# Optimization experiments

Hardware: AMD Instinct MI355X
Metric: run time of the kernel (lower is better)

## Reference

```python
import jax, jax.numpy as jnp
import numpy as np

B, IN, OUT, N, K = 2048, 4096, 4096, 64, 4  # batch, in_features, out_features, num_nodes, degree


def setup_inputs() -> dict:
    key = jax.random.key(0)
    k0, k1, k2, k3 = jax.random.split(key, 4)
    x = jax.random.normal(k0, (B, IN), dtype=jnp.float32)
    # kaiming-ish init for the linear weight
    W = jax.random.normal(k1, (OUT, IN), dtype=jnp.float32) * (1.0 / np.sqrt(IN))
    ecoeff = jax.random.uniform(k2, (N, N), dtype=jnp.float32, minval=0.1, maxval=0.5)
    phase = jax.random.uniform(k3, (N, N), dtype=jnp.float32, minval=0.0, maxval=2.0 * np.pi)
    tension = jnp.ones((N,), dtype=jnp.float32)
    # deterministic degree-K ring topology: paths[i] = [(i+1..i+K) % N]
    src = jnp.repeat(jnp.arange(N), K).astype(jnp.int32)            # [E]
    dst = ((src + jnp.tile(jnp.arange(1, K + 1), N)) % N).astype(jnp.int32)  # [E]
    return {"x": x, "W": W, "ecoeff": ecoeff, "phase": phase,
            "tension": tension, "src": src, "dst": dst}


def reference(x, W, ecoeff, phase, tension, src, dst):
    # EntangledConnectionLayer.forward
    b = x.shape[0]
    out_features = W.shape[0]
    n = tension.shape[0]
    opn = out_features // n  # out_per_node

    out = x @ W.T  # [B, OUT] == F.linear(x, weights)
    nodes = out.reshape(b, n, opn)  # [B, N, opn] node-sliced view of output

    # entangled_connection_function on a real signal:
    # real(sig * (1 + eps*exp(i*phi)) / (1 + tau_i*tau_j)) = sig*(1+eps*cos(phi))/(1+tau_i*tau_j)
    eps = ecoeff[src, dst]                    # [E]
    phi = phase[src, dst]                     # [E]
    tau = tension[src] * tension[dst]         # [E]
    scale = (1.0 + eps * jnp.cos(phi)) / (1.0 + tau)  # [E]

    contrib = nodes[:, src, :] * scale[None, :, None]  # [B, E, opn]
    entangled = jnp.zeros_like(nodes).at[:, dst, :].add(contrib)  # scatter-add over edges

    return out + 0.5 * entangled.reshape(b, out_features)
```

## Files before the change

### kernel.cpp

```cpp
#include <hip/hip_runtime.h>
#include <hip/hip_bf16.h>

#define TILE 128
#define BK 64

typedef __attribute__((ext_vector_type(8))) short bf16x8;
typedef __attribute__((ext_vector_type(4))) float f32x4;

__device__ __forceinline__ unsigned short f32_to_bf16(float f) {
    unsigned u = __float_as_uint(f);
    unsigned rounded = u + 0x7FFF + ((u >> 16) & 1);
    return (unsigned short)(rounded >> 16);
}
__device__ __forceinline__ float bf16_to_f32(unsigned short h) {
    return __uint_as_float(((unsigned)h) << 16);
}
__device__ __forceinline__ bool probe_f32(const void* tens) {
    return ((const unsigned short*)tens)[0] == 0;
}

__global__ __launch_bounds__(256)
void cast_x_kernel(const void* __restrict__ xv, unsigned short* __restrict__ xo,
                   const void* __restrict__ tens)
{
    const bool isF32 = probe_f32(tens);
    const size_t i = ((size_t)blockIdx.x * 256 + threadIdx.x) * 8;
    if (isF32) {
        const float4 a = *(const float4*)((const float*)xv + i);
        const float4 b = *(const float4*)((const float*)xv + i + 4);
        unsigned short p[8];
        p[0]=f32_to_bf16(a.x); p[1]=f32_to_bf16(a.y); p[2]=f32_to_bf16(a.z); p[3]=f32_to_bf16(a.w);
        p[4]=f32_to_bf16(b.x); p[5]=f32_to_bf16(b.y); p[6]=f32_to_bf16(b.z); p[7]=f32_to_bf16(b.w);
        *(bf16x8*)(xo + i) = *(const bf16x8*)p;
    } else {
        *(bf16x8*)(xo + i) = *(const bf16x8*)((const unsigned short*)xv + i);
    }
}

__global__ __launch_bounds__(256)
void wprime_kernel(const void* __restrict__ Wv,
                   const void* __restrict__ ecoeff, const void* __restrict__ phase,
                   const void* __restrict__ tens,
                   const int* __restrict__ srcIdx, const int* __restrict__ dstIdx,
                   unsigned short* __restrict__ Wp, int E, int K)
{
    constexpr int NODES = 64, CHUNK = 128, CAP = 8;
    __shared__ float buf[NODES * CHUNK];
    __shared__ int   cnt[NODES];
    __shared__ int   slist[NODES * CAP];
    __shared__ float clist[NODES * CAP];

    const bool isF32 = probe_f32(tens);
    const int tid = threadIdx.x;
    const int j   = blockIdx.x;
    const int k0  = blockIdx.y * CHUNK;

    if (tid < NODES) cnt[tid] = 0;
    __syncthreads();
    if (tid < E) {
        const int s = srcIdx[tid];
        const int d = dstIdx[tid];
        float eps, phi, ts, td;
        if (isF32) {
            eps = ((const float*)ecoeff)[s * NODES + d];
            phi = ((const float*)phase)[s * NODES + d];
            ts  = ((const float*)tens)[s];
            td  = ((const float*)tens)[d];
        } else {
            eps = bf16_to_f32(((const unsigned short*)ecoeff)[s * NODES + d]);
            phi = bf16_to_f32(((const unsigned short*)phase)[s * NODES + d]);
            ts  = bf16_to_f32(((const unsigned short*)tens)[s]);
            td  = bf16_to_f32(((const unsigned short*)tens)[d]);
        }
        const float coef = 0.5f * (1.0f + eps * __cosf(phi)) / (1.0f + ts * td);
        const int pos = atomicAdd(&cnt[d], 1);
        if (pos < CAP) { slist[d * CAP + pos] = s; clist[d * CAP + pos] = coef; }
    }

    if (isF32) {
        for (int idx = tid; idx < NODES * CHUNK / 4; idx += 256) {
            const int s = idx >> 5;
            const int p = idx & 31;
            const float4 v = *(const float4*)
                ((const float*)Wv + ((size_t)(s * 64 + j)) * K + k0 + p * 4);
            *(float4*)&buf[s * CHUNK + p * 4] = v;
        }
    } else {
        for (int idx = tid; idx < NODES * CHUNK / 4; idx += 256) {
            const int s = idx >> 5;
            const int p = idx & 31;
            const ushort4 v = *(const ushort4*)
                ((const unsigned short*)Wv + ((size_t)(s * 64 + j)) * K + k0 + p * 4);
            buf[s * CHUNK + p * 4 + 0] = bf16_to_f32(v.x);
            buf[s * CHUNK + p * 4 + 1] = bf16_to_f32(v.y);
            buf[s * CHUNK + p * 4 + 2] = bf16_to_f32(v.z);
            buf[s * CHUNK + p * 4 + 3] = bf16_to_f32(v.w);
        }
    }
    __syncthreads();

    const int kk = tid & (CHUNK - 1);
    const int dh = (tid >> 7) * 32;
#pragma unroll 4
    for (int dd = 0; dd < 32; ++dd) {
        const int d = dh + dd;
        float v = buf[d * CHUNK + kk];
        const int n = cnt[d] < CAP ? cnt[d] : CAP;
        for (int t = 0; t < n; ++t)
            v += clist[d * CAP + t] * buf[slist[d * CAP + t] * CHUNK + kk];
        Wp[((size_t)(d * 64 + j)) * K + k0 + kk] = f32_to_bf16(v);
    }
}

__global__ __launch_bounds__(256)
void gemm_ws_kernel(const unsigned short* __restrict__ A,
                    const unsigned short* __restrict__ B,
                    void* __restrict__ Cv, const void* __restrict__ tens,
                    int M, int N, int K)
{
    __shared__ __align__(16) unsigned short As[TILE * BK];
    __shared__ __align__(16) unsigned short Bs[TILE * BK];

    const bool isF32 = probe_f32(tens);
    const int tid  = threadIdx.x;
    const int lane = tid & 63;
    const int w    = tid >> 6;
    const int wm   = (w >> 1) * 64;
    const int wn   = (w & 1) * 64;
    const int m0   = blockIdx.y * TILE;
    const int n0   = blockIdx.x * TILE;

    f32x4 acc[4][4] = {};

    const int lrow = lane >> 3;
    const int lcol = (lane & 7) * 8;

    for (int k0 = 0; k0 < K; k0 += BK) {
#pragma unroll
        for (int t = 0; t < 4; ++t) {
            const int br = t * 32 + w * 8;
            const unsigned short* ga = A + (size_t)(m0 + br + lrow) * K + (k0 + lcol);
            const unsigned short* gb = B + (size_t)(n0 + br + lrow) * K + (k0 + lcol);
            __builtin_amdgcn_global_load_lds(
                (__attribute__((address_space(1))) const void*)ga,
                (__attribute__((address_space(3))) void*)&As[br * BK], 16, 0, 0);
            __builtin_amdgcn_global_load_lds(
                (__attribute__((address_space(1))) const void*)gb,
                (__attribute__((address_space(3))) void*)&Bs[br * BK], 16, 0, 0);
        }
        __syncthreads();

#pragma unroll
        for (int kk = 0; kk < BK; kk += 32) {
            const int rk = kk + (lane >> 4) * 8;
            const int rr = lane & 15;
            bf16x8 av[4], bv[4];
#pragma unroll
            for (int i = 0; i < 4; ++i)
                av[i] = *(const bf16x8*)&As[(wm + i * 16 + rr) * BK + rk];
#pragma unroll
            for (int i = 0; i < 4; ++i)
                bv[i] = *(const bf16x8*)&Bs[(wn + i * 16 + rr) * BK + rk];
#pragma unroll
            for (int mt = 0; mt < 4; ++mt)
#pragma unroll
                for (int nt = 0; nt < 4; ++nt)
                    acc[mt][nt] = __builtin_amdgcn_mfma_f32_16x16x32_bf16(
                        av[mt], bv[nt], acc[mt][nt], 0, 0, 0);
        }
        __syncthreads();
    }

    const int quad = (lane >> 4) * 4;
    const int col  = lane & 15;
#pragma unroll
    for (int mt = 0; mt < 4; ++mt)
#pragma unroll
        for (int nt = 0; nt < 4; ++nt)
#pragma unroll
            for (int r = 0; r < 4; ++r) {
                const size_t gr = (size_t)(m0 + wm + mt * 16 + quad + r);
                const size_t gc = (size_t)(n0 + wn + nt * 16 + col);
                const float v = acc[mt][nt][r];
                if (isF32) ((float*)Cv)[gr * N + gc] = v;
                else       ((unsigned short*)Cv)[gr * N + gc] = f32_to_bf16(v);
            }
}

__global__ __launch_bounds__(256)
void gemm_bt_kernel(const void* __restrict__ Av, const void* __restrict__ Bv,
                    void* __restrict__ Cv, const void* __restrict__ tens,
                    int M, int N, int K)
{
    __shared__ __align__(16) short As[TILE * BK];
    __shared__ __align__(16) short Bs[TILE * BK];

    const bool isF32 = probe_f32(tens);
    const int tid  = threadIdx.x;
    const int lane = tid & 63;
    const int w    = tid >> 6;
    const int wm   = (w >> 1) * 64;
    const int wn   = (w & 1) * 64;
    const int m0   = blockIdx.y * TILE;
    const int n0   = blockIdx.x * TILE;
    f32x4 acc[4][4] = {};
    const int lrow = lane >> 3;
    const int lcol = (lane & 7) * 8;

    for (int k0 = 0; k0 < K; k0 += BK) {
        if (!isF32) {
            const short* A = (const short*)Av;
            const short* B = (const short*)Bv;
#pragma unroll
            for (int t = 0; t < 4; ++t) {
                const int br = t * 32 + w * 8;
                const short* ga = A + (size_t)(m0 + br + lrow) * K + (k0 + lcol);
                const short* gb = B + (size_t)(n0 + br + lrow) * K + (k0 + lcol);
                __builtin_amdgcn_global_load_lds(
                    (__attribute__((address_space(1))) const void*)ga,
                    (__attribute__((address_space(3))) void*)&As[br * BK], 16, 0, 0);
                __builtin_amdgcn_global_load_lds(
                    (__attribute__((address_space(1))) const void*)gb,
                    (__attribute__((address_space(3))) void*)&Bs[br * BK], 16, 0, 0);
            }
        } else {
            const float* A = (const float*)Av;
            const float* B = (const float*)Bv;
#pragma unroll
            for (int t = 0; t < 4; ++t) {
                const int br = t * 32 + w * 8;
                const int row = br + lrow;
                const float* ga = A + (size_t)(m0 + row) * K + (k0 + lcol);
                const float* gb = B + (size_t)(n0 + row) * K + (k0 + lcol);
                float4 a0 = *(const float4*)(ga);
                float4 a1 = *(const float4*)(ga + 4);
                float4 b0 = *(const float4*)(gb);
                float4 b1 = *(const float4*)(gb + 4);
                short pa[8], pb[8];
                pa[0]=f32_to_bf16(a0.x); pa[1]=f32_to_bf16(a0.y);
                pa[2]=f32_to_bf16(a0.z); pa[3]=f32_to_bf16(a0.w);
                pa[4]=f32_to_bf16(a1.x); pa[5]=f32_to_bf16(a1.y);
                pa[6]=f32_to_bf16(a1.z); pa[7]=f32_to_bf16(a1.w);
                pb[0]=f32_to_bf16(b0.x); pb[1]=f32_to_bf16(b0.y);
                pb[2]=f32_to_bf16(b0.z); pb[3]=f32_to_bf16(b0.w);
                pb[4]=f32_to_bf16(b1.x); pb[5]=f32_to_bf16(b1.y);
                pb[6]=f32_to_bf16(b1.z); pb[7]=f32_to_bf16(b1.w);
                *(bf16x8*)&As[row * BK + lcol] = *(const bf16x8*)pa;
                *(bf16x8*)&Bs[row * BK + lcol] = *(const bf16x8*)pb;
            }
        }
        __syncthreads();
#pragma unroll
        for (int kk = 0; kk < BK; kk += 32) {
            const int rk = kk + (lane >> 4) * 8;
            const int rr = lane & 15;
            bf16x8 av[4], bv[4];
#pragma unroll
            for (int i = 0; i < 4; ++i)
                av[i] = *(const bf16x8*)&As[(wm + i * 16 + rr) * BK + rk];
#pragma unroll
            for (int i = 0; i < 4; ++i)
                bv[i] = *(const bf16x8*)&Bs[(wn + i * 16 + rr) * BK + rk];
#pragma unroll
            for (int mt = 0; mt < 4; ++mt)
#pragma unroll
                for (int nt = 0; nt < 4; ++nt)
                    acc[mt][nt] = __builtin_amdgcn_mfma_f32_16x16x32_bf16(
                        av[mt], bv[nt], acc[mt][nt], 0, 0, 0);
        }
        __syncthreads();
    }
    const int quad = (lane >> 4) * 4;
    const int col  = lane & 15;
#pragma unroll
    for (int mt = 0; mt < 4; ++mt)
#pragma unroll
        for (int nt = 0; nt < 4; ++nt)
#pragma unroll
            for (int r = 0; r < 4; ++r) {
                const size_t gr = (size_t)(m0 + wm + mt * 16 + quad + r);
                const size_t gc = (size_t)(n0 + wn + nt * 16 + col);
                const float v = acc[mt][nt][r];
                if (isF32) ((float*)Cv)[gr * N + gc] = v;
                else       ((unsigned short*)Cv)[gr * N + gc] = f32_to_bf16(v);
            }
}

__global__ __launch_bounds__(256)
void entangle_kernel(void* __restrict__ Cv,
                     const void* __restrict__ ecoeff,
                     const void* __restrict__ phase,
                     const void* __restrict__ tens,
                     const int* __restrict__ srcIdx,
                     const int* __restrict__ dstIdx,
                     int E)
{
    constexpr int NODES = 64, OPN = 64, FEAT = 4096, ROWS = 2, CAP = 8;
    __shared__ float rows[ROWS * FEAT];
    __shared__ int   cnt[NODES];
    __shared__ int   slist[NODES * CAP];
    __shared__ float clist[NODES * CAP];

    const bool isF32 = probe_f32(tens);
    const int tid = threadIdx.x;
    if (tid < NODES) cnt[tid] = 0;
    __syncthreads();

    if (tid < E) {
        const int s = srcIdx[tid];
        const int d = dstIdx[tid];
        float eps, phi, ts, td;
        if (isF32) {
            eps = ((const float*)ecoeff)[s * NODES + d];
            phi = ((const float*)phase)[s * NODES + d];
            ts  = ((const float*)tens)[s];
            td  = ((const float*)tens)[d];
        } else {
            eps = bf16_to_f32(((const unsigned short*)ecoeff)[s * NODES + d]);
            phi = bf16_to_f32(((const unsigned short*)phase)[s * NODES + d]);
            ts  = bf16_to_f32(((const unsigned short*)tens)[s]);
            td  = bf16_to_f32(((const unsigned short*)tens)[d]);
        }
        const float coef = 0.5f * (1.0f + eps * __cosf(phi)) / (1.0f + ts * td);
        const int pos = atomicAdd(&cnt[d], 1);
        if (pos < CAP) { slist[d * CAP + pos] = s; clist[d * CAP + pos] = coef; }
    }

    const size_t row0 = (size_t)blockIdx.x * ROWS;
    if (isF32) {
        const float4* g = (const float4*)((const float*)Cv + row0 * FEAT);
        float4* l = (float4*)rows;
        for (int i = tid; i < ROWS * FEAT / 4; i += 256) l[i] = g[i];
    } else {
        const ushort2* g = (const ushort2*)((const unsigned short*)Cv + row0 * FEAT);
        for (int i = tid; i < ROWS * FEAT / 2; i += 256) {
            const ushort2 u = g[i];
            rows[i * 2 + 0] = bf16_to_f32(u.x);
            rows[i * 2 + 1] = bf16_to_f32(u.y);
        }
    }
    __syncthreads();

    for (int c = 0; c < ROWS * FEAT / 256; ++c) {
        const int i = c * 256 + tid;
        const int r = i >> 12;
        const int o = i & (FEAT - 1);
        const int d = o >> 6;
        const int j = o & (OPN - 1);
        float v = rows[i];
        const int n = cnt[d] < CAP ? cnt[d] : CAP;
        for (int t = 0; t < n; ++t)
            v += clist[d * CAP + t] * rows[(r << 12) + slist[d * CAP + t] * OPN + j];
        if (isF32) ((float*)Cv)[(row0 + r) * FEAT + o] = v;
        else       ((unsigned short*)Cv)[(row0 + r) * FEAT + o] = f32_to_bf16(v);
    }
}

extern "C" void kernel_launch(void* const* d_in, const int* in_sizes, int n_in,
                              void* d_out, int out_size, void* d_ws, size_t ws_size,
                              hipStream_t stream)
{
    const void* x       = d_in[0];
    const void* W       = d_in[1];
    const void* ecoeff  = d_in[2];
    const void* phase   = d_in[3];
    const void* tension = d_in[4];
    const int*  src     = (const int*)d_in[5];
    const int*  dst     = (const int*)d_in[6];

    const int INF  = 4096;
    const int OUTF = 4096;
    const int M    = in_sizes[0] / INF;
    const int E    = in_sizes[5];

    dim3 grid(OUTF / TILE, M / TILE), block(256);
    const size_t needA = (size_t)M * INF * sizeof(unsigned short);
    const size_t needW = (size_t)OUTF * INF * sizeof(unsigned short);

    if (ws_size >= needA + needW) {
        unsigned short* xa = (unsigned short*)d_ws;
        unsigned short* wp = (unsigned short*)((char*)d_ws + needA);
        cast_x_kernel<<<dim3((M * INF) / (256 * 8)), block, 0, stream>>>(x, xa, tension);
        wprime_kernel<<<dim3(64, INF / 128), block, 0, stream>>>(
            W, ecoeff, phase, tension, src, dst, wp, E, INF);
        gemm_ws_kernel<<<grid, block, 0, stream>>>(xa, wp, d_out, tension, M, OUTF, INF);
    } else {
        gemm_bt_kernel<<<grid, block, 0, stream>>>(x, W, d_out, tension, M, OUTF, INF);
        entangle_kernel<<<dim3(M / 2), block, 0, stream>>>(
            d_out, ecoeff, phase, tension, src, dst, E);
    }
}
```

Before: 264.7 us.

## Fuse prep kernels, add split-K GEMM with atomics, swizzle LDS layout

Merges the x cast, W' construction and a new output-zeroing pass into one prep kernel launch. The GEMM is split along K into two halves on fp32 outputs, with results accumulated via atomicAdd into a zeroed output, to double the number of workgroups (512 instead of 256 tiles). LDS tiles now use an XOR swizzle on 16-byte columns to reduce bank conflicts on the MFMA operand reads. The risks are extra atomic traffic and zeroing writes on a 32 MB output, and run-to-run nondeterminism in float summation order.

Result: slower. 280.0 us (+5.8%).

```diff
diff --git a/kernel.cpp b/kernel.cpp
--- a/kernel.cpp
+++ b/kernel.cpp
@@ -20,29 +20,13 @@
 }
 
 __global__ __launch_bounds__(256)
-void cast_x_kernel(const void* __restrict__ xv, unsigned short* __restrict__ xo,
-                   const void* __restrict__ tens)
-{
-    const bool isF32 = probe_f32(tens);
-    const size_t i = ((size_t)blockIdx.x * 256 + threadIdx.x) * 8;
-    if (isF32) {
-        const float4 a = *(const float4*)((const float*)xv + i);
-        const float4 b = *(const float4*)((const float*)xv + i + 4);
-        unsigned short p[8];
-        p[0]=f32_to_bf16(a.x); p[1]=f32_to_bf16(a.y); p[2]=f32_to_bf16(a.z); p[3]=f32_to_bf16(a.w);
-        p[4]=f32_to_bf16(b.x); p[5]=f32_to_bf16(b.y); p[6]=f32_to_bf16(b.z); p[7]=f32_to_bf16(b.w);
-        *(bf16x8*)(xo + i) = *(const bf16x8*)p;
-    } else {
-        *(bf16x8*)(xo + i) = *(const bf16x8*)((const unsigned short*)xv + i);
-    }
-}
-
-__global__ __launch_bounds__(256)
-void wprime_kernel(const void* __restrict__ Wv,
-                   const void* __restrict__ ecoeff, const void* __restrict__ phase,
-                   const void* __restrict__ tens,
-                   const int* __restrict__ srcIdx, const int* __restrict__ dstIdx,
-                   unsigned short* __restrict__ Wp, int E, int K)
+void prep_kernel(const void* __restrict__ xv, const void* __restrict__ Wv,
+                 const void* __restrict__ ecoeff, const void* __restrict__ phase,
+                 const void* __restrict__ tens,
+                 const int* __restrict__ srcIdx, const int* __restrict__ dstIdx,
+                 unsigned short* __restrict__ xa, unsigned short* __restrict__ wp,
+                 void* __restrict__ outv, int E, int K, int outElems,
+                 int castB, int wpB, int zB)
 {
     constexpr int NODES = 64, CHUNK = 128, CAP = 8;
     __shared__ float buf[NODES * CHUNK];
@@ -52,76 +36,107 @@
 
     const bool isF32 = probe_f32(tens);
     const int tid = threadIdx.x;
-    const int j   = blockIdx.x;
-    const int k0  = blockIdx.y * CHUNK;
-
-    if (tid < NODES) cnt[tid] = 0;
-    __syncthreads();
-    if (tid < E) {
-        const int s = srcIdx[tid];
-        const int d = dstIdx[tid];
-        float eps, phi, ts, td;
+    const int b   = blockIdx.x;
+
+    if (b < castB) {
+        const size_t i = ((size_t)b * 256 + tid) * 8;
         if (isF32) {
-            eps = ((const float*)ecoeff)[s * NODES + d];
-            phi = ((const float*)phase)[s * NODES + d];
-            ts  = ((const float*)tens)[s];
-            td  = ((const float*)tens)[d];
+            const float4 a = *(const float4*)((const float*)xv + i);
+            const float4 c = *(const float4*)((const float*)xv + i + 4);
+            unsigned short p[8];
+            p[0]=f32_to_bf16(a.x); p[1]=f32_to_bf16(a.y); p[2]=f32_to_bf16(a.z); p[3]=f32_to_bf16(a.w);
+            p[4]=f32_to_bf16(c.x); p[5]=f32_to_bf16(c.y); p[6]=f32_to_bf16(c.z); p[7]=f32_to_bf16(c.w);
+            *(bf16x8*)(xa + i) = *(const bf16x8*)p;
         } else {
-            eps = bf16_to_f32(((const unsigned short*)ecoeff)[s * NODES + d]);
-            phi = bf16_to_f32(((const unsigned short*)phase)[s * NODES + d]);
-            ts  = bf16_to_f32(((const unsigned short*)tens)[s]);
-            td  = bf16_to_f32(((const unsigned short*)tens)[d]);
-        }
-        const float coef = 0.5f * (1.0f + eps * __cosf(phi)) / (1.0f + ts * td);
-        const int pos = atomicAdd(&cnt[d], 1);
-        if (pos < CAP) { slist[d * CAP + pos] = s; clist[d * CAP + pos] = coef; }
-    }
-
-    if (isF32) {
-        for (int idx = tid; idx < NODES * CHUNK / 4; idx += 256) {
-            const int s = idx >> 5;
-            const int p = idx & 31;
-            const float4 v = *(const float4*)
-                ((const float*)Wv + ((size_t)(s * 64 + j)) * K + k0 + p * 4);
-            *(float4*)&buf[s * CHUNK + p * 4] = v;
-        }
-    } else {
-        for (int idx = tid; idx < NODES * CHUNK / 4; idx += 256) {
-            const int s = idx >> 5;
-            const int p = idx & 31;
-            const ushort4 v = *(const ushort4*)
-                ((const unsigned short*)Wv + ((size_t)(s * 64 + j)) * K + k0 + p * 4);
-            buf[s * CHUNK + p * 4 + 0] = bf16_to_f32(v.x);
-            buf[s * CHUNK + p * 4 + 1] = bf16_to_f32(v.y);
-            buf[s * CHUNK + p * 4 + 2] = bf16_to_f32(v.z);
-            buf[s * CHUNK + p * 4 + 3] = bf16_to_f32(v.w);
-        }
-    }
-    __syncthreads();
-
-    const int kk = tid & (CHUNK - 1);
-    const int dh = (tid >> 7) * 32;
+            *(bf16x8*)(xa + i) = *(const bf16x8*)((const unsigned short*)xv + i);
+        }
+        return;
+    }
+    if (b < castB + wpB) {
+        const int wb = b - castB;
+        const int j  = wb & 63;
+        const int k0 = (wb >> 6) * CHUNK;
+
+        if (tid < NODES) cnt[tid] = 0;
+        __syncthreads();
+        if (tid < E) {
+            const int s = srcIdx[tid];
+            const int d = dstIdx[tid];
+            float eps, phi, ts, td;
+            if (isF32) {
+                eps = ((const float*)ecoeff)[s * NODES + d];
+                phi = ((const float*)phase)[s * NODES + d];
+                ts  = ((const float*)tens)[s];
+                td  = ((const float*)tens)[d];
+            } else {
+                eps = bf16_to_f32(((const unsigned short*)ecoeff)[s * NODES + d]);
+                phi = bf16_to_f32(((const unsigned short*)phase)[s * NODES + d]);
+                ts  = bf16_to_f32(((const unsigned short*)tens)[s]);
+                td  = bf16_to_f32(((const unsigned short*)tens)[d]);
+            }
+            const float coef = 0.5f * (1.0f + eps * __cosf(phi)) / (1.0f + ts * td);
+            const int pos = atomicAdd(&cnt[d], 1);
+            if (pos < CAP) { slist[d * CAP + pos] = s; clist[d * CAP + pos] = coef; }
+        }
+        if (isF32) {
+            for (int idx = tid; idx < NODES * CHUNK / 4; idx += 256) {
+                const int s = idx >> 5;
+                const int p = idx & 31;
+                const float4 v = *(const float4*)
+                    ((const float*)Wv + ((size_t)(s * 64 + j)) * K + k0 + p * 4);
+                *(float4*)&buf[s * CHUNK + p * 4] = v;
+            }
+        } else {
+            for (int idx = tid; idx < NODES * CHUNK / 4; idx += 256) {
+                const int s = idx >> 5;
+                const int p = idx & 31;
+                const ushort4 v = *(const ushort4*)
+                    ((const unsigned short*)Wv + ((size_t)(s * 64 + j)) * K + k0 + p * 4);
+                buf[s * CHUNK + p * 4 + 0] = bf16_to_f32(v.x);
+                buf[s * CHUNK + p * 4 + 1] = bf16_to_f32(v.y);
+                buf[s * CHUNK + p * 4 + 2] = bf16_to_f32(v.z);
+                buf[s * CHUNK + p * 4 + 3] = bf16_to_f32(v.w);
+            }
+        }
+        __syncthreads();
+
+        const int kk = tid & (CHUNK - 1);
+        const int dh = (tid >> 7) * 32;
 #pragma unroll 4
-    for (int dd = 0; dd < 32; ++dd) {
-        const int d = dh + dd;
-        float v = buf[d * CHUNK + kk];
-        const int n = cnt[d] < CAP ? cnt[d] : CAP;
-        for (int t = 0; t < n; ++t)
-            v += clist[d * CAP + t] * buf[slist[d * CAP + t] * CHUNK + kk];
-        Wp[((size_t)(d * 64 + j)) * K + k0 + kk] = f32_to_bf16(v);
+        for (int dd = 0; dd < 32; ++dd) {
+            const int d = dh + dd;
+            float v = buf[d * CHUNK + kk];
+            const int n = cnt[d] < CAP ? cnt[d] : CAP;
+            for (int t = 0; t < n; ++t)
+                v += clist[d * CAP + t] * buf[slist[d * CAP + t] * CHUNK + kk];
+            wp[((size_t)(d * 64 + j)) * K + k0 + kk] = f32_to_bf16(v);
+        }
+        return;
+    }
+    {
+        const int zb = b - castB - wpB;
+        const size_t byteOff = ((size_t)zb * 256 + tid) * 16;
+        const size_t total = (size_t)outElems * (isF32 ? 4 : 2);
+        if (byteOff < total) {
+            float4 z; z.x = 0.f; z.y = 0.f; z.z = 0.f; z.w = 0.f;
+            *(float4*)((char*)outv + byteOff) = z;
+        }
     }
 }
 
 __global__ __launch_bounds__(256)
-void gemm_ws_kernel(const unsigned short* __restrict__ A,
-                    const unsigned short* __restrict__ B,
-                    void* __restrict__ Cv, const void* __restrict__ tens,
-                    int M, int N, int K)
+void gemm_splitk_kernel(const unsigned short* __restrict__ A,
+                        const unsigned short* __restrict__ B,
+                        void* __restrict__ Cv, const void* __restrict__ tens,
+                        int M, int N, int K, int KS)
 {
     __shared__ __align__(16) unsigned short As[TILE * BK];
     __shared__ __align__(16) unsigned short Bs[TILE * BK];
 
     const bool isF32 = probe_f32(tens);
+    const int kz = blockIdx.z;
+    if (!isF32 && kz != 0) return;
+
     const int tid  = threadIdx.x;
     const int lane = tid & 63;
     const int w    = tid >> 6;
@@ -130,17 +145,20 @@
     const int m0   = blockIdx.y * TILE;
     const int n0   = blockIdx.x * TILE;
 
+    const int kbeg = isF32 ? kz * KS : 0;
+    const int kend = isF32 ? kbeg + KS : K;
+
     f32x4 acc[4][4] = {};
 
-    const int lrow = lane >> 3;
-    const int lcol = (lane & 7) * 8;
-
-    for (int k0 = 0; k0 < K; k0 += BK) {
+    const int lrow   = lane >> 3;
+    const int lcolsw = ((lane & 7) ^ lrow) * 8;
+
+    for (int k0 = kbeg; k0 < kend; k0 += BK) {
 #pragma unroll
         for (int t = 0; t < 4; ++t) {
             const int br = t * 32 + w * 8;
-            const unsigned short* ga = A + (size_t)(m0 + br + lrow) * K + (k0 + lcol);
-            const unsigned short* gb = B + (size_t)(n0 + br + lrow) * K + (k0 + lcol);
+            const unsigned short* ga = A + (size_t)(m0 + br + lrow) * K + (k0 + lcolsw);
+            const unsigned short* gb = B + (size_t)(n0 + br + lrow) * K + (k0 + lcolsw);
             __builtin_amdgcn_global_load_lds(
                 (__attribute__((address_space(1))) const void*)ga,
                 (__attribute__((address_space(3))) void*)&As[br * BK], 16, 0, 0);
@@ -152,15 +170,16 @@
 
 #pragma unroll
         for (int kk = 0; kk < BK; kk += 32) {
-            const int rk = kk + (lane >> 4) * 8;
             const int rr = lane & 15;
+            const int g  = (lane >> 4) + (kk >> 3);
+            const int slot = (g ^ (rr & 7)) * 8;
             bf16x8 av[4], bv[4];
 #pragma unroll
             for (int i = 0; i < 4; ++i)
-                av[i] = *(const bf16x8*)&As[(wm + i * 16 + rr) * BK + rk];
+                av[i] = *(const bf16x8*)&As[(wm + i * 16 + rr) * BK + slot];
 #pragma unroll
             for (int i = 0; i < 4; ++i)
-                bv[i] = *(const bf16x8*)&Bs[(wn + i * 16 + rr) * BK + rk];
+                bv[i] = *(const bf16x8*)&Bs[(wn + i * 16 + rr) * BK + slot];
 #pragma unroll
             for (int mt = 0; mt < 4; ++mt)
 #pragma unroll
@@ -182,7 +201,7 @@
                 const size_t gr = (size_t)(m0 + wm + mt * 16 + quad + r);
                 const size_t gc = (size_t)(n0 + wn + nt * 16 + col);
                 const float v = acc[mt][nt][r];
-                if (isF32) ((float*)Cv)[gr * N + gc] = v;
+                if (isF32) atomicAdd(&((float*)Cv)[gr * N + gc], v);
                 else       ((unsigned short*)Cv)[gr * N + gc] = f32_to_bf16(v);
             }
 }
@@ -373,18 +392,25 @@
     const int M    = in_sizes[0] / INF;
     const int E    = in_sizes[5];
 
-    dim3 grid(OUTF / TILE, M / TILE), block(256);
     const size_t needA = (size_t)M * INF * sizeof(unsigned short);
     const size_t needW = (size_t)OUTF * INF * sizeof(unsigned short);
 
     if (ws_size >= needA + needW) {
         unsigned short* xa = (unsigned short*)d_ws;
         unsigned short* wp = (unsigned short*)((char*)d_ws + needA);
-        cast_x_kernel<<<dim3((M * INF) / (256 * 8)), block, 0, stream>>>(x, xa, tension);
-        wprime_kernel<<<dim3(64, INF / 128), block, 0, stream>>>(
-            W, ecoeff, phase, tension, src, dst, wp, E, INF);
-        gemm_ws_kernel<<<grid, block, 0, stream>>>(xa, wp, d_out, tension, M, OUTF, INF);
+
+        const int castB = (M * INF) / (256 * 8);
+        const int wpB   = 64 * (INF / 128);
+        const int zB    = (int)(((size_t)out_size * 4 + 4095) / 4096);
+        prep_kernel<<<dim3(castB + wpB + zB), dim3(256), 0, stream>>>(
+            x, W, ecoeff, phase, tension, src, dst, xa, wp,
+            d_out, E, INF, out_size, castB, wpB, zB);
+
+        dim3 grid(OUTF / TILE, M / TILE, 2), block(256);
+        gemm_splitk_kernel<<<grid, block, 0, stream>>>(
+            xa, wp, d_out, tension, M, OUTF, INF, INF / 2);
     } else {
+        dim3 grid(OUTF / TILE, M / TILE), block(256);
         gemm_bt_kernel<<<grid, block, 0, stream>>>(x, W, d_out, tension, M, OUTF, INF);
         entangle_kernel<<<dim3(M / 2), block, 0, stream>>>(
             d_out, ecoeff, phase, tension, src, dst, E);
```

## Swizzle GEMM LDS layout and restructure W-prime build per destination node

Applied to the files above, without the earlier changes.

The GEMM now XOR-swizzles the 16-byte column slots of its LDS tiles, both on the global-to-LDS load and on the fragment reads, to cut LDS bank conflicts during the MFMA operand loads. The W' precompute kernel is rewritten so each block handles one destination node and four rows, reading source rows straight from global memory with float4 loads. This drops the 32KB shared staging buffer and the all-edges list. In exchange, source rows are re-read from global memory once per incoming edge, and the edge filter is recomputed in every block.

Result: faster. 252.7 us (-4.5%).

```diff
diff --git a/kernel.cpp b/kernel.cpp
--- a/kernel.cpp
+++ b/kernel.cpp
@@ -38,28 +38,26 @@
 }
 
 __global__ __launch_bounds__(256)
-void wprime_kernel(const void* __restrict__ Wv,
-                   const void* __restrict__ ecoeff, const void* __restrict__ phase,
-                   const void* __restrict__ tens,
-                   const int* __restrict__ srcIdx, const int* __restrict__ dstIdx,
-                   unsigned short* __restrict__ Wp, int E, int K)
-{
-    constexpr int NODES = 64, CHUNK = 128, CAP = 8;
-    __shared__ float buf[NODES * CHUNK];
-    __shared__ int   cnt[NODES];
-    __shared__ int   slist[NODES * CAP];
-    __shared__ float clist[NODES * CAP];
+void wprime_direct_kernel(const void* __restrict__ Wv,
+                          const void* __restrict__ ecoeff, const void* __restrict__ phase,
+                          const void* __restrict__ tens,
+                          const int* __restrict__ srcIdx, const int* __restrict__ dstIdx,
+                          unsigned short* __restrict__ Wp, int E, int K)
+{
+    constexpr int NODES = 64, CAP = 8;
+    __shared__ int   cnt;
+    __shared__ int   slist[CAP];
+    __shared__ float clist[CAP];
 
     const bool isF32 = probe_f32(tens);
     const int tid = threadIdx.x;
-    const int j   = blockIdx.x;
-    const int k0  = blockIdx.y * CHUNK;
-
-    if (tid < NODES) cnt[tid] = 0;
+    const int d   = blockIdx.x;
+    const int j0  = blockIdx.y * 4;
+
+    if (tid == 0) cnt = 0;
     __syncthreads();
-    if (tid < E) {
+    if (tid < E && dstIdx[tid] == d) {
         const int s = srcIdx[tid];
-        const int d = dstIdx[tid];
         float eps, phi, ts, td;
         if (isF32) {
             eps = ((const float*)ecoeff)[s * NODES + d];
@@ -73,42 +71,43 @@
             td  = bf16_to_f32(((const unsigned short*)tens)[d]);
         }
         const float coef = 0.5f * (1.0f + eps * __cosf(phi)) / (1.0f + ts * td);
-        const int pos = atomicAdd(&cnt[d], 1);
-        if (pos < CAP) { slist[d * CAP + pos] = s; clist[d * CAP + pos] = coef; }
-    }
-
-    if (isF32) {
-        for (int idx = tid; idx < NODES * CHUNK / 4; idx += 256) {
-            const int s = idx >> 5;
-            const int p = idx & 31;
-            const float4 v = *(const float4*)
-                ((const float*)Wv + ((size_t)(s * 64 + j)) * K + k0 + p * 4);
-            *(float4*)&buf[s * CHUNK + p * 4] = v;
-        }
-    } else {
-        for (int idx = tid; idx < NODES * CHUNK / 4; idx += 256) {
-            const int s = idx >> 5;
-            const int p = idx & 31;
-            const ushort4 v = *(const ushort4*)
-                ((const unsigned short*)Wv + ((size_t)(s * 64 + j)) * K + k0 + p * 4);
-            buf[s * CHUNK + p * 4 + 0] = bf16_to_f32(v.x);
-            buf[s * CHUNK + p * 4 + 1] = bf16_to_f32(v.y);
-            buf[s * CHUNK + p * 4 + 2] = bf16_to_f32(v.z);
-            buf[s * CHUNK + p * 4 + 3] = bf16_to_f32(v.w);
-        }
+        const int pos = atomicAdd(&cnt, 1);
+        if (pos < CAP) { slist[pos] = s; clist[pos] = coef; }
     }
     __syncthreads();
 
-    const int kk = tid & (CHUNK - 1);
-    const int dh = (tid >> 7) * 32;
-#pragma unroll 4
-    for (int dd = 0; dd < 32; ++dd) {
-        const int d = dh + dd;
-        float v = buf[d * CHUNK + kk];
-        const int n = cnt[d] < CAP ? cnt[d] : CAP;
-        for (int t = 0; t < n; ++t)
-            v += clist[d * CAP + t] * buf[slist[d * CAP + t] * CHUNK + kk];
-        Wp[((size_t)(d * 64 + j)) * K + k0 + kk] = f32_to_bf16(v);
+    const int n  = cnt < CAP ? cnt : CAP;
+    const int j  = j0 + (tid >> 6);
+    const int k0 = (tid & 63) * 4;
+    const size_t rowD = (size_t)(d * 64 + j) * K;
+
+    for (int k = k0; k < K; k += 256) {
+        float v0, v1, v2, v3;
+        if (isF32) {
+            const float4 a = *(const float4*)((const float*)Wv + rowD + k);
+            v0 = a.x; v1 = a.y; v2 = a.z; v3 = a.w;
+            for (int t = 0; t < n; ++t) {
+                const float c = clist[t];
+                const float4 b = *(const float4*)
+                    ((const float*)Wv + (size_t)(slist[t] * 64 + j) * K + k);
+                v0 += c * b.x; v1 += c * b.y; v2 += c * b.z; v3 += c * b.w;
+            }
+        } else {
+            const ushort4 a = *(const ushort4*)((const unsigned short*)Wv + rowD + k);
+            v0 = bf16_to_f32(a.x); v1 = bf16_to_f32(a.y);
+            v2 = bf16_to_f32(a.z); v3 = bf16_to_f32(a.w);
+            for (int t = 0; t < n; ++t) {
+                const float c = clist[t];
+                const ushort4 b = *(const ushort4*)
+                    ((const unsigned short*)Wv + (size_t)(slist[t] * 64 + j) * K + k);
+                v0 += c * bf16_to_f32(b.x); v1 += c * bf16_to_f32(b.y);
+                v2 += c * bf16_to_f32(b.z); v3 += c * bf16_to_f32(b.w);
+            }
+        }
+        ushort4 o;
+        o.x = f32_to_bf16(v0); o.y = f32_to_bf16(v1);
+        o.z = f32_to_bf16(v2); o.w = f32_to_bf16(v3);
+        *(ushort4*)(Wp + rowD + k) = o;
     }
 }
 
@@ -132,15 +131,15 @@
 
     f32x4 acc[4][4] = {};
 
-    const int lrow = lane >> 3;
-    const int lcol = (lane & 7) * 8;
+    const int lrow   = lane >> 3;
+    const int lcolsw = ((lane & 7) ^ lrow) * 8;
 
     for (int k0 = 0; k0 < K; k0 += BK) {
 #pragma unroll
         for (int t = 0; t < 4; ++t) {
             const int br = t * 32 + w * 8;
-            const unsigned short* ga = A + (size_t)(m0 + br + lrow) * K + (k0 + lcol);
-            const unsigned short* gb = B + (size_t)(n0 + br + lrow) * K + (k0 + lcol);
+            const unsigned short* ga = A + (size_t)(m0 + br + lrow) * K + (k0 + lcolsw);
+            const unsigned short* gb = B + (size_t)(n0 + br + lrow) * K + (k0 + lcolsw);
             __builtin_amdgcn_global_load_lds(
                 (__attribute__((address_space(1))) const void*)ga,
                 (__attribute__((address_space(3))) void*)&As[br * BK], 16, 0, 0);
@@ -152,15 +151,16 @@
 
 #pragma unroll
         for (int kk = 0; kk < BK; kk += 32) {
-            const int rk = kk + (lane >> 4) * 8;
             const int rr = lane & 15;
+            const int g  = (lane >> 4) + (kk >> 3);
+            const int slot = (g ^ (rr & 7)) * 8;
             bf16x8 av[4], bv[4];
 #pragma unroll
             for (int i = 0; i < 4; ++i)
-                av[i] = *(const bf16x8*)&As[(wm + i * 16 + rr) * BK + rk];
+                av[i] = *(const bf16x8*)&As[(wm + i * 16 + rr) * BK + slot];
 #pragma unroll
             for (int i = 0; i < 4; ++i)
-                bv[i] = *(const bf16x8*)&Bs[(wn + i * 16 + rr) * BK + rk];
+                bv[i] = *(const bf16x8*)&Bs[(wn + i * 16 + rr) * BK + slot];
 #pragma unroll
             for (int mt = 0; mt < 4; ++mt)
 #pragma unroll
@@ -373,18 +373,20 @@
     const int M    = in_sizes[0] / INF;
     const int E    = in_sizes[5];
 
-    dim3 grid(OUTF / TILE, M / TILE), block(256);
     const size_t needA = (size_t)M * INF * sizeof(unsigned short);
     const size_t needW = (size_t)OUTF * INF * sizeof(unsigned short);
 
     if (ws_size >= needA + needW) {
         unsigned short* xa = (unsigned short*)d_ws;
         unsigned short* wp = (unsigned short*)((char*)d_ws + needA);
-        cast_x_kernel<<<dim3((M * INF) / (256 * 8)), block, 0, stream>>>(x, xa, tension);
-        wprime_kernel<<<dim3(64, INF / 128), block, 0, stream>>>(
+
+        cast_x_kernel<<<dim3((M * INF) / (256 * 8)), dim3(256), 0, stream>>>(x, xa, tension);
+        wprime_direct_kernel<<<dim3(64, 16), dim3(256), 0, stream>>>(
             W, ecoeff, phase, tension, src, dst, wp, E, INF);
-        gemm_ws_kernel<<<grid, block, 0, stream>>>(xa, wp, d_out, tension, M, OUTF, INF);
+        gemm_ws_kernel<<<dim3(OUTF / TILE, M / TILE), dim3(256), 0, stream>>>(
+            xa, wp, d_out, tension, M, OUTF, INF);
     } else {
+        dim3 grid(OUTF / TILE, M / TILE), block(256);
         gemm_bt_kernel<<<grid, block, 0, stream>>>(x, W, d_out, tension, M, OUTF, INF);
         entangle_kernel<<<dim3(M / 2), block, 0, stream>>>(
             d_out, ecoeff, phase, tension, src, dst, E);
```
